# Optimization experiments

Measured on AMD Instinct MI355X. Metric: run time of the kernel, lower is better.

The kernel has to match this reference:

```python
import jax, jax.numpy as jnp
import numpy as np

B, N, D, H, DA, DL = 8, 1024, 512, 8, 64, 64
U_DIM = DL * H * 3          # 1536: u channel (3 attention channels worth)
NB = 128                    # timestamp-delta buckets
HID = 4 * D                 # FFN hidden (ffn_multiply=4)
EPS = 1e-6


def _rms(x):
    return x * jax.lax.rsqrt(jnp.mean(x * x, axis=-1, keepdims=True) + EPS)


def setup_inputs() -> dict:
    key = jax.random.key(0)
    ks = jax.random.split(key, 12)
    L = N // 2
    total = B * L
    x_offsets = jnp.arange(B + 1, dtype=jnp.int32) * L
    x = jax.random.normal(ks[0], (total, D), jnp.float32)
    all_timestamps = jnp.sort(jax.random.randint(ks[1], (B, N), 0, 1_000_000, dtype=jnp.int64), axis=1)
    invalid_attn_mask = jnp.tril(jnp.ones((N, N), jnp.float32))
    uvqk = jax.random.normal(ks[2], (D, DL * H * 4 + DA * H * 2), jnp.float32) * 0.02
    pos_w = jax.random.normal(ks[3], (2 * N - 1,), jnp.float32) * 0.02
    ts_w = jax.random.normal(ks[4], (NB,), jnp.float32) * 0.02
    W0 = jax.random.normal(ks[5], (U_DIM, D), jnp.float32) * (1.0 / np.sqrt(U_DIM))
    b0 = jnp.zeros((D,), jnp.float32)
    W1 = jax.random.normal(ks[6], (D, HID), jnp.float32) * (1.0 / np.sqrt(D))
    W2 = jax.random.normal(ks[7], (HID, D), jnp.float32) * (1.0 / np.sqrt(HID))
    W3 = jax.random.normal(ks[8], (D, HID), jnp.float32) * (1.0 / np.sqrt(D))
    return dict(x=x, x_offsets=x_offsets, all_timestamps=all_timestamps,
                invalid_attn_mask=invalid_attn_mask, uvqk=uvqk, pos_w=pos_w,
                ts_w=ts_w, W0=W0, b0=b0, W1=W1, W2=W2, W3=W3)


def reference(x, x_offsets, all_timestamps, invalid_attn_mask, uvqk, pos_w, ts_w, W0, b0, W1, W2, W3):
    total = x.shape[0]
    tok = jnp.arange(total)
    b_idx = jnp.searchsorted(x_offsets, tok, side='right') - 1   # batch id per jagged token
    p_idx = tok - x_offsets[b_idx]                               # position within sequence

    # input RMSNorm + fused uvqk projection with SiLU
    normed = _rms(x)
    mm = jax.nn.silu(normed @ uvqk)
    u, v, q, k = jnp.split(mm, [U_DIM, U_DIM + DL * H, U_DIM + DL * H + DA * H], axis=1)

    def pad(vals):  # jagged_to_padded_dense
        return jnp.zeros((B, N, vals.shape[-1]), vals.dtype).at[b_idx, p_idx].set(vals)

    pq = pad(q).reshape(B, N, H, DA)
    pk = pad(k).reshape(B, N, H, DA)
    pv = pad(v).reshape(B, N, H, DL)

    # channel 1: content-content SiLU attention
    qk_attn = jax.nn.silu(jnp.einsum('bnhd,bmhd->bhnm', pq, pk)) / N
    qk_attn = qk_attn * invalid_attn_mask[None, None]

    # channel 2: relative positional bias (shared across batch)
    rel = jnp.arange(N)[:, None] - jnp.arange(N)[None, :] + (N - 1)
    pos_attn = pos_w[rel] * invalid_attn_mask                     # (N, N)

    # channel 3: log-bucketed relative temporal bias
    dt = all_timestamps[:, :, None] - all_timestamps[:, None, :]
    bucket = jnp.clip(jnp.floor(jnp.log(jnp.abs(dt).astype(jnp.float32) + 1.0)).astype(jnp.int32), 0, NB - 1)
    ts_attn = ts_w[bucket] * invalid_attn_mask[None]              # (B, N, N)

    out_pos = jnp.einsum('nm,bmhd->bnhd', pos_attn, pv)
    out_ts = jnp.einsum('bnm,bmhd->bnhd', ts_attn, pv)
    out_lat = jnp.einsum('bhnm,bmhd->bnhd', qk_attn, pv)
    combined = jnp.concatenate([out_pos, out_ts, out_lat], axis=-1).reshape(B, N, U_DIM)
    attn_output = combined[b_idx, p_idx]                          # dense_to_jagged

    # AMS gating + multistage FFN with residuals
    ams = u * _rms(attn_output)
    X = ams @ W0 + b0 + x
    nX = _rms(X)
    X1 = jax.nn.silu(nX @ W1) * (nX @ W3)
    return X1 @ W2 + X
```

## Files before the change

kernel.cpp:

```cpp
#include <hip/hip_runtime.h>
#include <hip/hip_bf16.h>
#include <cstdint>
#include <cstddef>

typedef __hip_bfloat16 bf16;
typedef __attribute__((ext_vector_type(8))) short bf8v;
typedef __attribute__((ext_vector_type(4))) float f4v;
typedef __attribute__((ext_vector_type(4))) short s4v;
typedef __attribute__((ext_vector_type(8))) short s8v;

#define DEV static __device__ __forceinline__

DEV float siluf(float v){ return v / (1.0f + __expf(-v)); }
DEV short bfs(float f){ bf16 h = __float2bfloat16(f); return __builtin_bit_cast(short, h); }
DEV float b2f(short s){ return __builtin_bit_cast(float, (unsigned)((unsigned short)s) << 16); }

DEV void gload16(const bf16* g, bf16* l){
  __builtin_amdgcn_global_load_lds((const __attribute__((address_space(1))) void*)g,
                                   (__attribute__((address_space(3))) void*)l, 16, 0, 0);
}

template<int BN>
DEV void gemm_core(const bf16* __restrict__ A, int lda,
                   const bf16* __restrict__ Bt, int ldb,
                   int K, bf16* As, bf16* Bs, f4v (&acc)[4][4],
                   int bm, int bn, int k0)
{
  constexpr int NT = (BN==128)?256:128;
  const int t = threadIdx.x, w = t>>6, l = t&63;
  const int wr = (BN==128)?(w>>1):w;
  const int wc = (BN==128)?(w&1):0;
  const int lr = l&15, kb = l>>4;
#pragma unroll
  for (int i=0;i<4;i++)
#pragma unroll
    for (int j=0;j<4;j++) acc[i][j] = (f4v)(0.0f);

  for (int kt=k0; kt<k0+K; kt+=32){
    __syncthreads();
#pragma unroll
    for (int i=0;i<512/NT;i++){
      int lin = t + i*NT;
      gload16(A + (size_t)(bm + (lin>>2))*lda + kt + (lin&3)*8,
              As + (size_t)(w*64 + i*NT)*8);
    }
#pragma unroll
    for (int i=0;i<(BN*4)/NT;i++){
      int lin = t + i*NT;
      gload16(Bt + (size_t)(bn + (lin>>2))*ldb + kt + (lin&3)*8,
              Bs + (size_t)(w*64 + i*NT)*8);
    }
    __syncthreads();
    bf8v af[4], bfr[4];
#pragma unroll
    for (int i=0;i<4;i++) af[i]  = *(const bf8v*)(As + (wr*64 + i*16 + lr)*32 + kb*8);
#pragma unroll
    for (int j=0;j<4;j++) bfr[j] = *(const bf8v*)(Bs + (wc*64 + j*16 + lr)*32 + kb*8);
#pragma unroll
    for (int i=0;i<4;i++)
#pragma unroll
      for (int j=0;j<4;j++)
        acc[i][j] = __builtin_amdgcn_mfma_f32_16x16x32_bf16(af[i], bfr[j], acc[i][j], 0,0,0);
  }
}

DEV void gemm_core_n64(const bf16* __restrict__ A, int lda,
                       const bf16* __restrict__ Bt, int ldb,
                       int K, bf16* As, bf16* Bs, f4v (&acc)[4][2],
                       int bm, int bn, int k0)
{
  const int t = threadIdx.x, w = t>>6, l = t&63;
  const int wr = w>>1, wc = w&1, lr = l&15, kb = l>>4;
#pragma unroll
  for (int i=0;i<4;i++)
#pragma unroll
    for (int j=0;j<2;j++) acc[i][j] = (f4v)(0.0f);

  for (int kt=k0; kt<k0+K; kt+=32){
    __syncthreads();
#pragma unroll
    for (int i=0;i<2;i++){
      int lin = t + i*256;
      gload16(A + (size_t)(bm + (lin>>2))*lda + kt + (lin&3)*8,
              As + (size_t)(w*64 + i*256)*8);
    }
    gload16(Bt + (size_t)(bn + (t>>2))*ldb + kt + (t&3)*8,
            Bs + (size_t)(w*64)*8);
    __syncthreads();
    bf8v af[4], bfr[2];
#pragma unroll
    for (int i=0;i<4;i++) af[i]  = *(const bf8v*)(As + (wr*64 + i*16 + lr)*32 + kb*8);
#pragma unroll
    for (int j=0;j<2;j++) bfr[j] = *(const bf8v*)(Bs + (wc*32 + j*16 + lr)*32 + kb*8);
#pragma unroll
    for (int i=0;i<4;i++)
#pragma unroll
      for (int j=0;j<2;j++)
        acc[i][j] = __builtin_amdgcn_mfma_f32_16x16x32_bf16(af[i], bfr[j], acc[i][j], 0,0,0);
  }
}

#define EPI_LOOP(BN, ...) { \
  const int t_=threadIdx.x, w_=t_>>6, l_=t_&63; \
  const int wr_=(BN==128)?(w_>>1):w_, wc_=(BN==128)?(w_&1):0; \
  const int lr_=l_&15, kb_=l_>>4; \
  _Pragma("unroll") for (int i_=0;i_<4;i_++) \
  _Pragma("unroll") for (int j_=0;j_<4;j_++) \
  _Pragma("unroll") for (int r_=0;r_<4;r_++){ \
    const int row = bm + wr_*64 + i_*16 + kb_*4 + r_; \
    const int col = bn + wc_*64 + j_*16 + lr_; \
    float v = acc[i_][j_][r_]; \
    __VA_ARGS__; \
  } }


__global__ __launch_bounds__(256) void k_gemm1(const bf16* __restrict__ xn,
                                               const bf16* __restrict__ uvqkT,
                                               bf16* __restrict__ mm,
                                               bf16* __restrict__ vT){
  __shared__ __align__(16) bf16 As[128*32];
  __shared__ __align__(16) bf16 Bs[128*32];
  f4v acc[4][4];
  const int bm = blockIdx.x*128, bn = blockIdx.y*128;
  gemm_core<128>(xn, 512, uvqkT, 512, 512, As, Bs, acc, bm, bn, 0);
  const int t=threadIdx.x, w=t>>6, l=t&63;
  const int wr=w>>1, wc=w&1, lr=l&15, kb=l>>4;
  const bool isv = (bn >= 1536) && (bn < 2048);
#pragma unroll
  for (int i=0;i<4;i++)
#pragma unroll
  for (int j=0;j<4;j++){
    const int row0 = bm + wr*64 + i*16 + kb*4;
    const int col  = bn + wc*64 + j*16 + lr;
    if (!isv){
#pragma unroll
      for (int r=0;r<4;r++)
        mm[(size_t)(row0+r)*3072 + col] = __float2bfloat16(siluf(acc[i][j][r]));
    } else {
      s4v p;
#pragma unroll
      for (int r=0;r<4;r++) p[r] = bfs(siluf(acc[i][j][r]));
      const int b = row0 >> 9, m = row0 & 511;
      *(s4v*)(vT + ((size_t)b*512 + (col-1536))*512 + m) = p;
    }
  }
}

__global__ __launch_bounds__(256) void k_gemm_qk(const bf16* __restrict__ mm,
                                                 bf16* __restrict__ Plat){
  __shared__ __align__(16) bf16 As[128*32];
  __shared__ __align__(16) bf16 Bs[128*32];
  f4v acc[4][4];
  const int bm = blockIdx.x*128, bn = blockIdx.y*128;
  if (bn >= bm + 128) return;
  const int z = blockIdx.z, b = z>>3, h = z&7;
  const bf16* A  = mm + (size_t)b*512*3072 + 2048 + h*64;
  const bf16* Bt = mm + (size_t)b*512*3072 + 2560 + h*64;
  gemm_core<128>(A, 3072, Bt, 3072, 64, As, Bs, acc, bm, bn, 0);
  bf16* P = Plat + (size_t)z*512*512;
  EPI_LOOP(128, {
    float s = (row >= col) ? siluf(v)*(1.0f/1024.0f) : 0.0f;
    P[(size_t)row*512 + col] = __float2bfloat16(s);
  })
}

__global__ __launch_bounds__(256) void k_pv_lat(const bf16* __restrict__ Plat,
                                                const bf16* __restrict__ vT,
                                                bf16* __restrict__ comb){
  __shared__ __align__(16) bf16 As[128*32];
  __shared__ __align__(16) bf16 Bs[64*32];
  f4v acc[4][2];
  const int z = blockIdx.z, b = z>>3, h = z&7;
  const bf16* A  = Plat + (size_t)z*512*512;
  const bf16* Bt = vT + ((size_t)b*512 + h*64)*512;
  const int bm = blockIdx.x*128;
  gemm_core_n64(A, 512, Bt, 512, bm + 128, As, Bs, acc, bm, 0, 0);
  const int t=threadIdx.x, w=t>>6, l=t&63;
  const int wr=w>>1, wc=w&1, lr=l&15, kb=l>>4;
#pragma unroll
  for (int i=0;i<4;i++)
#pragma unroll
  for (int j=0;j<2;j++)
#pragma unroll
  for (int r=0;r<4;r++){
    const int row = bm + wr*64 + i*16 + kb*4 + r;
    const int col = wc*32 + j*16 + lr;
    comb[((size_t)b*512 + row)*1536 + h*192 + 128 + col] = __float2bfloat16(acc[i][j][r]);
  }
}

__global__ __launch_bounds__(256) void k_pv_posts(const bf16* __restrict__ Apos,
                                                  const bf16* __restrict__ Ats,
                                                  const bf16* __restrict__ vT,
                                                  bf16* __restrict__ comb){
  __shared__ __align__(16) bf16 As[128*32];
  __shared__ __align__(16) bf16 Bs[128*32];
  f4v acc[4][4];
  const int z = blockIdx.z, b = z>>1, ch = z&1;
  const bf16* A  = ch ? (Ats + (size_t)b*512*512) : Apos;
  const bf16* Bt = vT + (size_t)b*512*512;
  const int bm = blockIdx.x*128, bn = blockIdx.y*128;
  gemm_core<128>(A, 512, Bt, 512, bm + 128, As, Bs, acc, bm, bn, 0);
  EPI_LOOP(128, comb[((size_t)b*512 + row)*1536 + (col>>6)*192 + ch*64 + (col&63)]
                    = __float2bfloat16(v); )
}

__global__ __launch_bounds__(256) void k_gemm_w0_sk(const bf16* __restrict__ ams,
                                                    const bf16* __restrict__ W0T,
                                                    float* __restrict__ parts){
  __shared__ __align__(16) bf16 As[128*32];
  __shared__ __align__(16) bf16 Bs[128*32];
  f4v acc[4][4];
  const int bm = blockIdx.x*128, bn = blockIdx.y*128, k0 = blockIdx.z*384;
  gemm_core<128>(ams, 1536, W0T, 1536, 384, As, Bs, acc, bm, bn, k0);
  float* P = parts + (size_t)blockIdx.z*4096*512;
  EPI_LOOP(128, P[(size_t)row*512 + col] = v; )
}

__global__ __launch_bounds__(128) void k_reduce_w0_rms(const float* __restrict__ parts,
                                                       const float* __restrict__ x,
                                                       const float* __restrict__ b0,
                                                       float* __restrict__ X,
                                                       bf16* __restrict__ nX){
  __shared__ float sbuf[16];
  const size_t row = blockIdx.x;
  const int t = threadIdx.x;
  float4 s = ((const float4*)(x + row*512))[t];
  const float4 bv = ((const float4*)b0)[t];
  s.x += bv.x; s.y += bv.y; s.z += bv.z; s.w += bv.w;
#pragma unroll
  for (int p=0;p<4;p++){
    const float4 pv = ((const float4*)(parts + (size_t)p*4096*512 + row*512))[t];
    s.x += pv.x; s.y += pv.y; s.z += pv.z; s.w += pv.w;
  }
  ((float4*)(X + row*512))[t] = s;
  float ss = s.x*s.x + s.y*s.y + s.z*s.z + s.w*s.w;
#pragma unroll
  for (int o=32;o>0;o>>=1) ss += __shfl_down(ss, o);
  const int ln = t & 63, wv = t >> 6;
  if (ln==0) sbuf[wv] = ss;
  __syncthreads();
  if (t==0) sbuf[8] = rsqrtf((sbuf[0]+sbuf[1])*(1.0f/512.0f) + 1e-6f);
  __syncthreads();
  const float r = sbuf[8];
  s4v o; o[0]=bfs(s.x*r); o[1]=bfs(s.y*r); o[2]=bfs(s.z*r); o[3]=bfs(s.w*r);
  ((s4v*)(nX + row*512))[t] = o;
}

__global__ __launch_bounds__(256) void k_gemm_w13f(const bf16* __restrict__ nX,
                                                   const bf16* __restrict__ W1T,
                                                   const bf16* __restrict__ W3T,
                                                   bf16* __restrict__ X1){
  __shared__ __align__(16) bf16 As[128*32];
  __shared__ __align__(16) bf16 Bs1[64*32];
  __shared__ __align__(16) bf16 Bs3[64*32];
  f4v a1[4][2], a3[4][2];
  const int bm = blockIdx.x*128, bn = blockIdx.y*64;
  const int t = threadIdx.x, w = t>>6, l = t&63;
  const int wr = w>>1, wc = w&1, lr = l&15, kb = l>>4;
#pragma unroll
  for (int i=0;i<4;i++)
#pragma unroll
    for (int j=0;j<2;j++){ a1[i][j] = (f4v)(0.0f); a3[i][j] = (f4v)(0.0f); }

  for (int kt=0; kt<512; kt+=32){
    __syncthreads();
#pragma unroll
    for (int i=0;i<2;i++){
      int lin = t + i*256;
      gload16(nX + (size_t)(bm + (lin>>2))*512 + kt + (lin&3)*8, As + (size_t)(w*64 + i*256)*8);
    }
    gload16(W1T + (size_t)(bn + (t>>2))*512 + kt + (t&3)*8, Bs1 + (size_t)(w*64)*8);
    gload16(W3T + (size_t)(bn + (t>>2))*512 + kt + (t&3)*8, Bs3 + (size_t)(w*64)*8);
    __syncthreads();
    bf8v af[4], b1[2], b3[2];
#pragma unroll
    for (int i=0;i<4;i++) af[i] = *(const bf8v*)(As + (wr*64 + i*16 + lr)*32 + kb*8);
#pragma unroll
    for (int j=0;j<2;j++){ b1[j] = *(const bf8v*)(Bs1 + (wc*32 + j*16 + lr)*32 + kb*8);
                           b3[j] = *(const bf8v*)(Bs3 + (wc*32 + j*16 + lr)*32 + kb*8); }
#pragma unroll
    for (int i=0;i<4;i++)
#pragma unroll
      for (int j=0;j<2;j++){
        a1[i][j] = __builtin_amdgcn_mfma_f32_16x16x32_bf16(af[i], b1[j], a1[i][j], 0,0,0);
        a3[i][j] = __builtin_amdgcn_mfma_f32_16x16x32_bf16(af[i], b3[j], a3[i][j], 0,0,0);
      }
  }
#pragma unroll
  for (int i=0;i<4;i++)
#pragma unroll
  for (int j=0;j<2;j++)
#pragma unroll
  for (int r=0;r<4;r++){
    const int row = bm + wr*64 + i*16 + kb*4 + r;
    const int col = bn + wc*32 + j*16 + lr;
    X1[(size_t)row*2048 + col] = __float2bfloat16(siluf(a1[i][j][r]) * a3[i][j][r]);
  }
}

__global__ __launch_bounds__(256) void k_gemm_w2_sk(const bf16* __restrict__ X1,
                                                    const bf16* __restrict__ W2T,
                                                    float* __restrict__ parts){
  __shared__ __align__(16) bf16 As[128*32];
  __shared__ __align__(16) bf16 Bs[128*32];
  f4v acc[4][4];
  const int bm = blockIdx.x*128, bn = blockIdx.y*128, k0 = blockIdx.z*512;
  gemm_core<128>(X1, 2048, W2T, 2048, 512, As, Bs, acc, bm, bn, k0);
  float* P = parts + (size_t)blockIdx.z*4096*512;
  EPI_LOOP(128, P[(size_t)row*512 + col] = v; )
}

__global__ __launch_bounds__(256) void k_reduce_w2(const float* __restrict__ parts,
                                                   float* __restrict__ out){
  const int i = blockIdx.x*256 + threadIdx.x;
  float4 s = ((const float4*)out)[i];
#pragma unroll
  for (int p=0;p<4;p++){
    const float4 pv = ((const float4*)(parts + (size_t)p*4096*512))[i];
    s.x += pv.x; s.y += pv.y; s.z += pv.z; s.w += pv.w;
  }
  ((float4*)out)[i] = s;
}


__global__ __launch_bounds__(192) void k_rms_mul_u(const bf16* __restrict__ comb,
                                                   const bf16* __restrict__ mm,
                                                   bf16* __restrict__ ams){
  __shared__ float sbuf[16];
  const size_t rb = (size_t)blockIdx.x;
  const s8v cv = ((const s8v*)(comb + rb*1536))[threadIdx.x];
  float cf[8]; float ss = 0.f;
#pragma unroll
  for (int j=0;j<8;j++){ cf[j] = b2f(cv[j]); ss += cf[j]*cf[j]; }
#pragma unroll
  for (int o=32;o>0;o>>=1) ss += __shfl_down(ss, o);
  const int ln = threadIdx.x & 63, wv = threadIdx.x >> 6;
  if (ln==0) sbuf[wv] = ss;
  __syncthreads();
  if (threadIdx.x==0) sbuf[8] = rsqrtf((sbuf[0]+sbuf[1]+sbuf[2])*(1.0f/1536.0f) + 1e-6f);
  __syncthreads();
  const float r = sbuf[8];
  const s8v uv = ((const s8v*)(mm + rb*3072))[threadIdx.x];
  s8v o;
#pragma unroll
  for (int j=0;j<8;j++) o[j] = bfs(b2f(uv[j]) * cf[j] * r);
  ((s8v*)(ams + rb*1536))[threadIdx.x] = o;
}

__global__ __launch_bounds__(256) void k_prep(
    const float* __restrict__ x,    const int* __restrict__ ts,
    const float* __restrict__ pos_w,const float* __restrict__ ts_w,
    const float* __restrict__ uvqk, const float* __restrict__ W0,
    const float* __restrict__ W1,   const float* __restrict__ W3,
    const float* __restrict__ W2,
    bf16* __restrict__ xn,
    bf16* __restrict__ uvqkT, bf16* __restrict__ W0T,
    bf16* __restrict__ W13T,  bf16* __restrict__ W2T,
    bf16* __restrict__ Apos,  bf16* __restrict__ Ats){
  __shared__ float tile[32][33];
  __shared__ float sbuf[16];
  int id = blockIdx.x;
  if (id < 5376){
    const float* src; bf16* dst; int R, C;
    if      (id < 1536){            src=uvqk; dst=uvqkT;                  R=512;  C=3072; }
    else if (id < 2304){ id-=1536;  src=W0;   dst=W0T;                    R=1536; C=512;  }
    else if (id < 3328){ id-=2304;  src=W1;   dst=W13T;                   R=512;  C=2048; }
    else if (id < 4352){ id-=3328;  src=W3;   dst=W13T+(size_t)2048*512;  R=512;  C=2048; }
    else               { id-=4352;  src=W2;   dst=W2T;                    R=2048; C=512;  }
    const int nbx = C >> 5;
    const int c0 = (id % nbx)*32, r0 = (id / nbx)*32;
    const int tx = threadIdx.x & 31, ty = threadIdx.x >> 5;
#pragma unroll
    for (int i=0;i<32;i+=8) tile[ty+i][tx] = src[(size_t)(r0+ty+i)*C + (c0+tx)];
    __syncthreads();
#pragma unroll
    for (int i=0;i<32;i+=8) dst[(size_t)(c0+ty+i)*R + (r0+tx)] = __float2bfloat16(tile[tx][ty+i]);
  } else if (id < 14592){
    int id2 = id - 5376;
    const int mblk = id2 & 1, n = (id2>>1)&511, z = id2>>10;
    if (mblk*256 > n) return;
    const int m = mblk*256 + threadIdx.x;
    if (z == 0){
      float v = (n >= m) ? pos_w[n - m + 1023] : 0.f;
      Apos[(size_t)n*512 + m] = __float2bfloat16(v);
    } else {
      const int b = z-1;
      int dt = ts[b*1024 + n] - ts[b*1024 + m];
      float ad = (float)(dt < 0 ? -dt : dt);
      int bucket = (int)floorf(logf(ad + 1.0f));
      bucket = bucket < 0 ? 0 : (bucket > 127 ? 127 : bucket);
      float v = (n >= m) ? ts_w[bucket] : 0.f;
      Ats[((size_t)b*512 + n)*512 + m] = __float2bfloat16(v);
    }
  } else {
    const size_t row = id - 14592;
    const int t = threadIdx.x;
    if (t >= 128) return;
    const float4 v = ((const float4*)(x + row*512))[t];
    float ss = v.x*v.x + v.y*v.y + v.z*v.z + v.w*v.w;
#pragma unroll
    for (int o=32;o>0;o>>=1) ss += __shfl_down(ss, o);
    const int ln = t & 63, wv = t >> 6;
    if (ln==0) sbuf[wv] = ss;
    __syncthreads();
    if (t==0) sbuf[8] = rsqrtf((sbuf[0]+sbuf[1])*(1.0f/512.0f) + 1e-6f);
    __syncthreads();
    const float r = sbuf[8];
    s4v o; o[0]=bfs(v.x*r); o[1]=bfs(v.y*r); o[2]=bfs(v.z*r); o[3]=bfs(v.w*r);
    ((s4v*)(xn + row*512))[t] = o;
  }
}


extern "C" void kernel_launch(void* const* d_in, const int* in_sizes, int n_in,
                              void* d_out, int out_size, void* d_ws, size_t ws_size,
                              hipStream_t stream) {
  const float* x     = (const float*)d_in[0];
  const int*   ts    = (const int*)d_in[2];
  const float* uvqk  = (const float*)d_in[4];
  const float* pos_w = (const float*)d_in[5];
  const float* ts_w  = (const float*)d_in[6];
  const float* W0    = (const float*)d_in[7];
  const float* b0    = (const float*)d_in[8];
  const float* W1    = (const float*)d_in[9];
  const float* W2    = (const float*)d_in[10];
  const float* W3    = (const float*)d_in[11];
  float* out = (float*)d_out;

  char* w = (char*)d_ws;
  auto alloc = [&](size_t bytes){ char* p = w; w += (bytes + 255) & ~(size_t)255; return p; };
  bf16*  xn    = (bf16*)alloc((size_t)4096*512*2);
  bf16*  uvqkT = (bf16*)alloc((size_t)3072*512*2);
  bf16*  W0T   = (bf16*)alloc((size_t)512*1536*2);
  bf16*  W13T  = (bf16*)alloc((size_t)4096*512*2);
  bf16*  W2T   = (bf16*)alloc((size_t)512*2048*2);
  bf16*  mm    = (bf16*)alloc((size_t)4096*3072*2);
  bf16*  vT    = (bf16*)alloc((size_t)8*512*512*2);
  bf16*  Apos  = (bf16*)alloc((size_t)512*512*2);
  bf16*  Ats   = (bf16*)alloc((size_t)8*512*512*2);
  bf16*  Plat  = (bf16*)alloc((size_t)64*512*512*2);
  bf16*  comb  = (bf16*)alloc((size_t)4096*1536*2);
  bf16*  ams   = (bf16*)alloc((size_t)4096*1536*2);
  bf16*  nX    = (bf16*)alloc((size_t)4096*512*2);
  float* parts = (float*)alloc((size_t)4*4096*512*4);
  bf16* X1 = Plat;

  k_prep<<<18688, 256, 0, stream>>>(x, ts, pos_w, ts_w, uvqk, W0, W1, W3, W2,
                                    xn, uvqkT, W0T, W13T, W2T, Apos, Ats);
  k_gemm1<<<dim3(32, 24), 256, 0, stream>>>(xn, uvqkT, mm, vT);
  k_gemm_qk<<<dim3(4, 4, 64), 256, 0, stream>>>(mm, Plat);
  k_pv_lat<<<dim3(4, 1, 64), 256, 0, stream>>>(Plat, vT, comb);
  k_pv_posts<<<dim3(4, 4, 16), 256, 0, stream>>>(Apos, Ats, vT, comb);
  k_rms_mul_u<<<4096, 192, 0, stream>>>(comb, mm, ams);
  k_gemm_w0_sk<<<dim3(32, 4, 4), 256, 0, stream>>>(ams, W0T, parts);
  k_reduce_w0_rms<<<4096, 128, 0, stream>>>(parts, x, b0, out, nX);
  k_gemm_w13f<<<dim3(32, 32), 256, 0, stream>>>(nX, W13T, W13T + (size_t)2048*512, X1);
  k_gemm_w2_sk<<<dim3(32, 4, 4), 256, 0, stream>>>(X1, W2T, parts);
  k_reduce_w2<<<2048, 256, 0, stream>>>(parts, out);
}
```

Before: 173.6 us.

## Fuse latent QK scoring and PV product into one flash-style attention kernel

Replaces the separate QK-score kernel, which wrote a 64x512x512 bf16 probability matrix to global memory, and the PV kernel that read it back, with one kernel. Each block keeps its Q tile in LDS, loops over causal K/V tiles, applies SiLU and the causal mask into an LDS score tile, and accumulates P·V in registers. This removes the global round trip of the score matrix and one launch. In exchange the grid shrinks to 256 blocks with uneven causal work per block, and LDS use per block grows.

```diff
diff --git a/kernel.cpp b/kernel.cpp
--- a/kernel.cpp
+++ b/kernel.cpp
@@ -60,42 +60,6 @@
     for (int i=0;i<4;i++)
 #pragma unroll
       for (int j=0;j<4;j++)
-        acc[i][j] = __builtin_amdgcn_mfma_f32_16x16x32_bf16(af[i], bfr[j], acc[i][j], 0,0,0);
-  }
-}
-
-DEV void gemm_core_n64(const bf16* __restrict__ A, int lda,
-                       const bf16* __restrict__ Bt, int ldb,
-                       int K, bf16* As, bf16* Bs, f4v (&acc)[4][2],
-                       int bm, int bn, int k0)
-{
-  const int t = threadIdx.x, w = t>>6, l = t&63;
-  const int wr = w>>1, wc = w&1, lr = l&15, kb = l>>4;
-#pragma unroll
-  for (int i=0;i<4;i++)
-#pragma unroll
-    for (int j=0;j<2;j++) acc[i][j] = (f4v)(0.0f);
-
-  for (int kt=k0; kt<k0+K; kt+=32){
-    __syncthreads();
-#pragma unroll
-    for (int i=0;i<2;i++){
-      int lin = t + i*256;
-      gload16(A + (size_t)(bm + (lin>>2))*lda + kt + (lin&3)*8,
-              As + (size_t)(w*64 + i*256)*8);
-    }
-    gload16(Bt + (size_t)(bn + (t>>2))*ldb + kt + (t&3)*8,
-            Bs + (size_t)(w*64)*8);
-    __syncthreads();
-    bf8v af[4], bfr[2];
-#pragma unroll
-    for (int i=0;i<4;i++) af[i]  = *(const bf8v*)(As + (wr*64 + i*16 + lr)*32 + kb*8);
-#pragma unroll
-    for (int j=0;j<2;j++) bfr[j] = *(const bf8v*)(Bs + (wc*32 + j*16 + lr)*32 + kb*8);
-#pragma unroll
-    for (int i=0;i<4;i++)
-#pragma unroll
-      for (int j=0;j<2;j++)
         acc[i][j] = __builtin_amdgcn_mfma_f32_16x16x32_bf16(af[i], bfr[j], acc[i][j], 0,0,0);
   }
 }
@@ -146,37 +110,93 @@
   }
 }
 
-__global__ __launch_bounds__(256) void k_gemm_qk(const bf16* __restrict__ mm,
-                                                 bf16* __restrict__ Plat){
-  __shared__ __align__(16) bf16 As[128*32];
-  __shared__ __align__(16) bf16 Bs[128*32];
-  f4v acc[4][4];
-  const int bm = blockIdx.x*128, bn = blockIdx.y*128;
-  if (bn >= bm + 128) return;
-  const int z = blockIdx.z, b = z>>3, h = z&7;
-  const bf16* A  = mm + (size_t)b*512*3072 + 2048 + h*64;
-  const bf16* Bt = mm + (size_t)b*512*3072 + 2560 + h*64;
-  gemm_core<128>(A, 3072, Bt, 3072, 64, As, Bs, acc, bm, bn, 0);
-  bf16* P = Plat + (size_t)z*512*512;
-  EPI_LOOP(128, {
-    float s = (row >= col) ? siluf(v)*(1.0f/1024.0f) : 0.0f;
-    P[(size_t)row*512 + col] = __float2bfloat16(s);
-  })
-}
-
-__global__ __launch_bounds__(256) void k_pv_lat(const bf16* __restrict__ Plat,
-                                                const bf16* __restrict__ vT,
-                                                bf16* __restrict__ comb){
-  __shared__ __align__(16) bf16 As[128*32];
-  __shared__ __align__(16) bf16 Bs[64*32];
-  f4v acc[4][2];
-  const int z = blockIdx.z, b = z>>3, h = z&7;
-  const bf16* A  = Plat + (size_t)z*512*512;
-  const bf16* Bt = vT + ((size_t)b*512 + h*64)*512;
+__global__ __launch_bounds__(256) void k_attn_lat(const bf16* __restrict__ mm,
+                                                  const bf16* __restrict__ vT,
+                                                  bf16* __restrict__ comb){
+  __shared__ __align__(16) bf16 Qs[2*128*32];
+  __shared__ __align__(16) bf16 Ks[2*128*32];
+  __shared__ __align__(16) bf16 Vs[4*64*32];
+  __shared__ __align__(16) bf16 Ss[4*128*32];
   const int bm = blockIdx.x*128;
-  gemm_core_n64(A, 512, Bt, 512, bm + 128, As, Bs, acc, bm, 0, 0);
-  const int t=threadIdx.x, w=t>>6, l=t&63;
-  const int wr=w>>1, wc=w&1, lr=l&15, kb=l>>4;
+  const int z = blockIdx.y, b = z>>3, h = z&7;
+  const int t = threadIdx.x, w = t>>6, l = t&63;
+  const int wr = w>>1, wc = w&1, lr = l&15, kb = l>>4;
+  const bf16* Qg = mm + (size_t)b*512*3072 + 2048 + h*64;
+  const bf16* Kg = mm + (size_t)b*512*3072 + 2560 + h*64;
+  const bf16* Vg = vT + ((size_t)b*512 + h*64)*512;
+  f4v o[4][2];
+#pragma unroll
+  for (int i=0;i<4;i++)
+#pragma unroll
+    for (int j=0;j<2;j++) o[i][j] = (f4v)(0.0f);
+
+#pragma unroll
+  for (int p=0;p<4;p++){
+    int s = t + p*256;
+    gload16(Qg + (size_t)(bm + ((s>>2)&127))*3072 + (s>>9)*32 + (s&3)*8,
+            Qs + (size_t)(w*64 + p*256)*8);
+  }
+  for (int bn=0; bn<=bm; bn+=128){
+    __syncthreads();
+#pragma unroll
+    for (int p=0;p<4;p++){
+      int s = t + p*256;
+      gload16(Kg + (size_t)(bn + ((s>>2)&127))*3072 + (s>>9)*32 + (s&3)*8,
+              Ks + (size_t)(w*64 + p*256)*8);
+    }
+#pragma unroll
+    for (int p=0;p<4;p++){
+      int s = t + p*256;
+      gload16(Vg + (size_t)((s>>2)&63)*512 + bn + (s>>8)*32 + (s&3)*8,
+              Vs + (size_t)(w*64 + p*256)*8);
+    }
+    __syncthreads();
+    f4v sacc[4][4];
+#pragma unroll
+    for (int i=0;i<4;i++)
+#pragma unroll
+      for (int j=0;j<4;j++) sacc[i][j] = (f4v)(0.0f);
+#pragma unroll
+    for (int ki=0; ki<2; ki++){
+      bf8v af[4], bk[4];
+#pragma unroll
+      for (int i=0;i<4;i++) af[i] = *(const bf8v*)(Qs + ki*4096 + (wr*64+i*16+lr)*32 + kb*8);
+#pragma unroll
+      for (int j=0;j<4;j++) bk[j] = *(const bf8v*)(Ks + ki*4096 + (wc*64+j*16+lr)*32 + kb*8);
+#pragma unroll
+      for (int i=0;i<4;i++)
+#pragma unroll
+        for (int j=0;j<4;j++)
+          sacc[i][j] = __builtin_amdgcn_mfma_f32_16x16x32_bf16(af[i], bk[j], sacc[i][j], 0,0,0);
+    }
+    const bool diag = (bn == bm);
+#pragma unroll
+    for (int i=0;i<4;i++)
+#pragma unroll
+    for (int j=0;j<4;j++)
+#pragma unroll
+    for (int r=0;r<4;r++){
+      const int row = wr*64 + i*16 + kb*4 + r;
+      const int col = wc*64 + j*16 + lr;
+      float sv = siluf(sacc[i][j][r])*(1.0f/1024.0f);
+      if (diag && row < col) sv = 0.0f;
+      Ss[(col>>5)*4096 + row*32 + (col&31)] = __float2bfloat16(sv);
+    }
+    __syncthreads();
+#pragma unroll
+    for (int kt=0; kt<4; kt++){
+      bf8v af[4], bv[2];
+#pragma unroll
+      for (int i=0;i<4;i++) af[i] = *(const bf8v*)(Ss + kt*4096 + (wr*64+i*16+lr)*32 + kb*8);
+#pragma unroll
+      for (int j=0;j<2;j++) bv[j] = *(const bf8v*)(Vs + kt*2048 + (wc*32+j*16+lr)*32 + kb*8);
+#pragma unroll
+      for (int i=0;i<4;i++)
+#pragma unroll
+        for (int j=0;j<2;j++)
+          o[i][j] = __builtin_amdgcn_mfma_f32_16x16x32_bf16(af[i], bv[j], o[i][j], 0,0,0);
+    }
+  }
 #pragma unroll
   for (int i=0;i<4;i++)
 #pragma unroll
@@ -185,7 +205,7 @@
   for (int r=0;r<4;r++){
     const int row = bm + wr*64 + i*16 + kb*4 + r;
     const int col = wc*32 + j*16 + lr;
-    comb[((size_t)b*512 + row)*1536 + h*192 + 128 + col] = __float2bfloat16(acc[i][j][r]);
+    comb[((size_t)b*512 + row)*1536 + h*192 + 128 + col] = __float2bfloat16(o[i][j][r]);
   }
 }
 
@@ -439,18 +459,16 @@
   bf16*  vT    = (bf16*)alloc((size_t)8*512*512*2);
   bf16*  Apos  = (bf16*)alloc((size_t)512*512*2);
   bf16*  Ats   = (bf16*)alloc((size_t)8*512*512*2);
-  bf16*  Plat  = (bf16*)alloc((size_t)64*512*512*2);
+  bf16*  X1    = (bf16*)alloc((size_t)4096*2048*2);
   bf16*  comb  = (bf16*)alloc((size_t)4096*1536*2);
   bf16*  ams   = (bf16*)alloc((size_t)4096*1536*2);
   bf16*  nX    = (bf16*)alloc((size_t)4096*512*2);
   float* parts = (float*)alloc((size_t)4*4096*512*4);
-  bf16* X1 = Plat;
 
   k_prep<<<18688, 256, 0, stream>>>(x, ts, pos_w, ts_w, uvqk, W0, W1, W3, W2,
                                     xn, uvqkT, W0T, W13T, W2T, Apos, Ats);
   k_gemm1<<<dim3(32, 24), 256, 0, stream>>>(xn, uvqkT, mm, vT);
-  k_gemm_qk<<<dim3(4, 4, 64), 256, 0, stream>>>(mm, Plat);
-  k_pv_lat<<<dim3(4, 1, 64), 256, 0, stream>>>(Plat, vT, comb);
+  k_attn_lat<<<dim3(4, 64), 256, 0, stream>>>(mm, vT, comb);
   k_pv_posts<<<dim3(4, 4, 16), 256, 0, stream>>>(Apos, Ats, vT, comb);
   k_rms_mul_u<<<4096, 192, 0, stream>>>(comb, mm, ams);
   k_gemm_w0_sk<<<dim3(32, 4, 4), 256, 0, stream>>>(ams, W0T, parts);
```

New measurement: 169.5 us. 2.4% less time.
